# Optimization experiments

Hardware: AMD Instinct MI355X
Metric: run time of the kernel (lower is better)

## Reference

```python
import jax, jax.numpy as jnp
import numpy as np

D_MODEL, FFN, N_EXP = 1024, 4096, 8
BS, L = 4, 2048


def setup_inputs() -> dict:
    key = jax.random.key(0)
    ks = jax.random.split(key, 7)
    s = 0.02
    return {
        "x": jax.random.normal(ks[0], (BS, L, D_MODEL), dtype=jnp.float32),
        "gate_w": s * jax.random.normal(ks[1], (D_MODEL, N_EXP), dtype=jnp.float32),
        "gate_b": jnp.zeros((N_EXP,), dtype=jnp.float32),
        "W1": s * jax.random.normal(ks[2], (N_EXP, D_MODEL, FFN), dtype=jnp.float32),
        "b1": jnp.zeros((N_EXP, FFN), dtype=jnp.float32),
        "W2": s * jax.random.normal(ks[3], (N_EXP, FFN, D_MODEL), dtype=jnp.float32),
        "b2": jnp.zeros((N_EXP, D_MODEL), dtype=jnp.float32),
    }


def reference(x, gate_w, gate_b, W1, b1, W2, b2):
    # gate logits [bs, l, E]; NOTE: original applies Softmax(dim=1) -> over seq dim
    logits = jnp.einsum("bld,de->ble", x, gate_w) + gate_b
    probs = jax.nn.softmax(logits, axis=1)  # faithful to nn.Softmax(dim=1)
    idx = jnp.argmax(probs, axis=-1)  # top-1 expert per token, [bs, l]
    # topk_weights are computed in the original but never applied to output.
    out = jnp.zeros_like(x)
    for e in range(N_EXP):  # fixed small expert loop (structurally distinct weights)
        h = jax.nn.gelu(jnp.einsum("bld,df->blf", x, W1[e]) + b1[e], approximate=False)
        y = jnp.einsum("blf,fd->bld", h, W2[e]) + b2[e]
        out = out + jnp.where((idx == e)[..., None], y, jnp.float32(0.0))
    return out
```

## Files before the change

### kernel.cpp

```cpp
#include <hip/hip_runtime.h>
#include <hip/hip_bf16.h>

typedef unsigned short u16;
typedef unsigned int u32;

using bf16x8 = __attribute__((ext_vector_type(8))) short;
using f32x4  = __attribute__((ext_vector_type(4))) float;

static constexpr int TOK  = 8192;
static constexpr int SEQ  = 2048;
static constexpr int DM   = 1024;
static constexpr int FF   = 4096;
static constexpr int NE   = 8;
static constexpr int MAXT = 72;
static constexpr int MAXT2= 40;
static constexpr int NT2  = DM/128;
static constexpr int KS2  = 2;
static constexpr int NWG1 = MAXT2 * (FF/256);
static constexpr int NWG2 = MAXT * NT2 * KS2;

static constexpr size_t O_LOGITS = 0;
static constexpr size_t O_M      = 262144;
static constexpr size_t O_Z      = O_M + 128;
static constexpr size_t O_CNT    = O_Z + 128;
static constexpr size_t O_CUR    = O_CNT + 64;
static constexpr size_t O_OFF    = O_CUR + 64;
static constexpr size_t O_DESC   = 263168;
static constexpr size_t O_DESC2  = 264320;
static constexpr size_t O_PERM   = 266240;
static constexpr size_t O_IDX    = 299008;
static constexpr size_t O_XG     = 524288;
static constexpr size_t O_W1T    = O_XG  + (size_t)TOK*DM*2;
static constexpr size_t O_W2T    = O_W1T + (size_t)NE*DM*FF*2;
static constexpr size_t O_H      = O_W2T + (size_t)NE*DM*FF*2;

__device__ __forceinline__ u16 f2bf(float f){
  __hip_bfloat16 h = __float2bfloat16(f);
  return *reinterpret_cast<u16*>(&h);
}

__device__ __forceinline__ void gld_lds16(const void* g, void* l){
  __builtin_amdgcn_global_load_lds((const __attribute__((address_space(1))) void*)g,
                                   (__attribute__((address_space(3))) void*)l, 16, 0, 0);
}

#define BAR()    asm volatile("s_barrier" ::: "memory")
#define WAITV0() asm volatile("s_waitcnt vmcnt(0)" ::: "memory")

__device__ __forceinline__ float gelu_f(float v){
  float u = v * fmaf(v*v, 0.044715f, 1.0f) * 0.7978845608f;
  float ex = __builtin_amdgcn_exp2f(u * -2.885390082f);
  return v * __builtin_amdgcn_rcpf(1.0f + ex);
}

__global__ void k_gate(const float* __restrict__ x, const float* __restrict__ gw,
                       const float* __restrict__ gb, float* __restrict__ logits){
  __shared__ float sgw[DM*NE];
  for (int i = threadIdx.x; i < DM*NE; i += 256) sgw[i] = gw[i];
  __syncthreads();
  int wave = threadIdx.x >> 6, lane = threadIdx.x & 63;
  int t = blockIdx.x * 4 + wave;
  const float* xr = x + (size_t)t * DM;
  float acc[NE];
#pragma unroll
  for (int e = 0; e < NE; ++e) acc[e] = 0.f;
#pragma unroll
  for (int k = 0; k < 16; ++k){
    int d = k*64 + lane;
    float xv = xr[d];
    const float* g = &sgw[d*NE];
#pragma unroll
    for (int e = 0; e < NE; ++e) acc[e] = fmaf(xv, g[e], acc[e]);
  }
#pragma unroll
  for (int off = 32; off; off >>= 1)
#pragma unroll
    for (int e = 0; e < NE; ++e) acc[e] += __shfl_xor(acc[e], off);
  if (lane == 0){
#pragma unroll
    for (int e = 0; e < NE; ++e) logits[(size_t)t*NE + e] = acc[e] + gb[e];
  }
}

__global__ void k_lse(const float* __restrict__ logits, float* __restrict__ mOut,
                      float* __restrict__ zOut){
  int be = blockIdx.x;
  int b = be >> 3, e = be & 7;
  const float* base = logits + ((size_t)b*SEQ)*NE + e;
  float m = -INFINITY;
  for (int l = threadIdx.x; l < SEQ; l += 256) m = fmaxf(m, base[(size_t)l*NE]);
  __shared__ float red[8];
#pragma unroll
  for (int off = 32; off; off >>= 1) m = fmaxf(m, __shfl_xor(m, off));
  if ((threadIdx.x & 63) == 0) red[threadIdx.x >> 6] = m;
  __syncthreads();
  m = fmaxf(fmaxf(red[0], red[1]), fmaxf(red[2], red[3]));
  float s = 0.f;
  for (int l = threadIdx.x; l < SEQ; l += 256) s += expf(base[(size_t)l*NE] - m);
#pragma unroll
  for (int off = 32; off; off >>= 1) s += __shfl_xor(s, off);
  if ((threadIdx.x & 63) == 0) red[4 + (threadIdx.x >> 6)] = s;
  __syncthreads();
  if (threadIdx.x == 0){ mOut[be] = m; zOut[be] = red[4]+red[5]+red[6]+red[7]; }
}

__global__ void k_route(const float* __restrict__ logits, const float* __restrict__ m,
                        const float* __restrict__ z, u32* __restrict__ cnt,
                        int* __restrict__ idx){
  int t = blockIdx.x*256 + threadIdx.x;
  int b = t >> 11;
  const float* lr = logits + (size_t)t*NE;
  float best = -INFINITY; int be = 0;
#pragma unroll
  for (int e = 0; e < NE; ++e){
    float p = expf(lr[e] - m[b*NE + e]) / z[b*NE + e];
    if (p > best){ best = p; be = e; }
  }
  idx[t] = be;
  atomicAdd(&cnt[be], 1u);
}

__global__ void k_plan(const u32* __restrict__ cnt, int* __restrict__ off,
                       int4* __restrict__ desc, int4* __restrict__ desc2,
                       u32* __restrict__ cur){
  if (threadIdx.x == 0){
    int offs[NE+1]; int o = 0;
    for (int e = 0; e < NE; ++e){ offs[e] = o; o += (int)cnt[e]; }
    offs[NE] = o;
    int nt = 0, nt2 = 0;
    for (int e = 0; e < NE; ++e){
      int c = (int)cnt[e];
      for (int s = 0; s < c; s += 128)
        desc[nt++] = make_int4(e, offs[e] + s, min(128, c - s), 0);
      for (int s = 0; s < c; s += 256)
        desc2[nt2++] = make_int4(e, offs[e] + s, min(256, c - s), 0);
      off[e] = offs[e]; cur[e] = 0u;
    }
    off[NE] = offs[NE];
    for (int i = nt;  i < MAXT;  ++i) desc[i]  = make_int4(-1, 0, 0, 0);
    for (int i = nt2; i < MAXT2; ++i) desc2[i] = make_int4(-1, 0, 0, 0);
  }
}

__global__ void k_scatter(const int* __restrict__ idx, const int* __restrict__ off,
                          u32* __restrict__ cur, int* __restrict__ perm){
  int t = blockIdx.x*256 + threadIdx.x;
  int e = idx[t];
  int pos = off[e] + (int)atomicAdd(&cur[e], 1u);
  perm[pos] = t;
}

__global__ void k_gather(const float* __restrict__ x, const int* __restrict__ perm,
                         u16* __restrict__ Xg){
  int p = blockIdx.x;
  int t = perm[p];
  const float4* src = (const float4*)(x + (size_t)t*DM);
  float4 v = src[threadIdx.x];
  uint2 o;
  o.x = (u32)f2bf(v.x) | ((u32)f2bf(v.y) << 16);
  o.y = (u32)f2bf(v.z) | ((u32)f2bf(v.w) << 16);
  *(uint2*)(Xg + (size_t)p*DM + threadIdx.x*4) = o;
}

__global__ void k_trans(const float* __restrict__ in, u16* __restrict__ out,
                        int R, int C){
  __shared__ float tile[64][65];
  int e = blockIdx.z;
  int r0 = blockIdx.x*64, c0 = blockIdx.y*64;
  const float* src = in + ((size_t)e*R + r0)*C + c0;
  int lr = threadIdx.x >> 4, lc = (threadIdx.x & 15) * 4;
#pragma unroll
  for (int i = 0; i < 4; ++i){
    float4 v = *(const float4*)(src + (size_t)(lr + i*16)*C + lc);
    tile[lr + i*16][lc+0] = v.x; tile[lr + i*16][lc+1] = v.y;
    tile[lr + i*16][lc+2] = v.z; tile[lr + i*16][lc+3] = v.w;
  }
  __syncthreads();
  u16* dst = out + ((size_t)e*C + c0)*R + r0;
#pragma unroll
  for (int i = 0; i < 4; ++i){
    int oc = lr + i*16;
    u16 a0 = f2bf(tile[lc+0][oc]);
    u16 a1 = f2bf(tile[lc+1][oc]);
    u16 a2 = f2bf(tile[lc+2][oc]);
    u16 a3 = f2bf(tile[lc+3][oc]);
    uint2 o; o.x = (u32)a0 | ((u32)a1 << 16); o.y = (u32)a2 | ((u32)a3 << 16);
    *(uint2*)(dst + (size_t)oc*R + lc) = o;
  }
}

__global__ __launch_bounds__(512, 2) void k_ffn1(const u16* __restrict__ Xg,
    const u16* __restrict__ W1T, const float* __restrict__ b1,
    u16* __restrict__ H, const int4* __restrict__ desc2){
  int pid = blockIdx.x;
  int pid_sw = (pid & 7) * (NWG1/8) + (pid >> 3);
  int mt = pid_sw % MAXT2;
  int n0 = (pid_sw / MAXT2) * 256;
  int4 dd = desc2[mt];
  int e = dd.x; if (e < 0) return;
  int m0 = dd.y, valid = dd.z;

  __shared__ __align__(16) u16 lA[2][256*64];
  __shared__ __align__(16) u16 lB[2][256*64];

  int tid = threadIdx.x, lane = tid & 63, wave = tid >> 6;
  int wm = wave >> 2, wn = wave & 3;
  const u16* Bsrc = W1T + ((size_t)e*FF + n0)*DM;

  f32x4 acc[8][4] = {};
  bf16x8 a[4][2], b0[2][2], b1r[2][2];

  int srow = lane >> 3;
  int cole = ((lane & 7) ^ srow) << 3;

  auto STAGE = [&](int buf, int kt){
    int k0 = kt * 64;
    char* dA = (char*)&lA[buf][0];
    char* dB = (char*)&lB[buf][0];
#pragma unroll
    for (int c = 0; c < 4; ++c){
      int ci = wave*4 + c;
      int row = ci*8 + srow;
      int ra = m0 + row; if (ra > TOK-1) ra = TOK-1;
      gld_lds16(Xg   + (size_t)ra *DM + k0 + cole, dA + ci*1024);
      gld_lds16(Bsrc + (size_t)row*DM + k0 + cole, dB + ci*1024);
    }
  };
  auto LDA = [&](const u16* tb, int half){
#pragma unroll
    for (int f = 0; f < 4; ++f){
      int R = wm*128 + half*64 + f*16 + (lane & 15);
      int base = R*128 + (((lane >> 4)*16) ^ ((R & 7) << 4));
      a[f][0] = *(const bf16x8*)((const char*)tb + base);
      a[f][1] = *(const bf16x8*)((const char*)tb + (base ^ 64));
    }
  };
  auto LDB = [&](const u16* tb, int half, bf16x8 (&b)[2][2]){
#pragma unroll
    for (int f = 0; f < 2; ++f){
      int R = wn*64 + half*32 + f*16 + (lane & 15);
      int base = R*128 + (((lane >> 4)*16) ^ ((R & 7) << 4));
      b[f][0] = *(const bf16x8*)((const char*)tb + base);
      b[f][1] = *(const bf16x8*)((const char*)tb + (base ^ 64));
    }
  };
  auto MM = [&](int mh, int nh, bf16x8 (&b)[2][2]){
    __builtin_amdgcn_s_setprio(1);
#pragma unroll
    for (int f = 0; f < 4; ++f)
#pragma unroll
      for (int g = 0; g < 2; ++g){
        acc[mh*4+f][nh*2+g] =
          __builtin_amdgcn_mfma_f32_16x16x32_bf16(a[f][0], b[g][0], acc[mh*4+f][nh*2+g], 0,0,0);
        acc[mh*4+f][nh*2+g] =
          __builtin_amdgcn_mfma_f32_16x16x32_bf16(a[f][1], b[g][1], acc[mh*4+f][nh*2+g], 0,0,0);
      }
    __builtin_amdgcn_s_setprio(0);
  };

  STAGE(0, 0);
  WAITV0(); BAR();
  const int KT = DM / 64;
  for (int kt = 0; kt < KT; ++kt){
    const u16* cA = &lA[kt & 1][0];
    const u16* cB = &lB[kt & 1][0];
    if (kt + 1 < KT) STAGE((kt & 1) ^ 1, kt + 1);
    LDA(cA, 0); LDB(cB, 0, b0);
    BAR(); MM(0, 0, b0);  BAR();
    LDB(cB, 1, b1r);
    BAR(); MM(0, 1, b1r); BAR();
    LDA(cA, 1);
    BAR(); MM(1, 1, b1r); BAR();
    MM(1, 0, b0);
    if (kt + 1 < KT) WAITV0();
    BAR();
  }

#pragma unroll
  for (int fn = 0; fn < 4; ++fn){
    int col = n0 + wn*64 + fn*16 + (lane & 15);
    float bias = b1[(size_t)e*FF + col];
#pragma unroll
    for (int fm = 0; fm < 8; ++fm){
      int rbase = wm*128 + fm*16 + ((lane >> 4) << 2);
#pragma unroll
      for (int j = 0; j < 4; ++j){
        int rit = rbase + j;
        if (rit < valid){
          float v = acc[fm][fn][j] + bias;
          H[(size_t)(m0 + rit)*FF + col] = f2bf(gelu_f(v));
        }
      }
    }
  }
}

__global__ void k_bias(const int* __restrict__ idx, const float* __restrict__ b2,
                       float* __restrict__ out){
  int t = blockIdx.x;
  int e = idx[t];
  float4 v = *(const float4*)(b2 + (size_t)e*DM + threadIdx.x*4);
  *(float4*)(out + (size_t)t*DM + threadIdx.x*4) = v;
}

__global__ __launch_bounds__(256) void k_ffn2(const u16* __restrict__ H,
    const u16* __restrict__ W2T, float* __restrict__ out,
    const int4* __restrict__ desc, const int* __restrict__ perm){
  int pid = blockIdx.x;
  int pid_sw = (pid & 7) * (NWG2/8) + (pid >> 3);
  int mt = pid_sw % MAXT;
  int rest = pid_sw / MAXT;
  int n0 = (rest & 7) * 128;
  int ks = rest >> 3;
  int4 dd = desc[mt];
  int e = dd.x; if (e < 0) return;
  int m0 = dd.y, valid = dd.z;
  __shared__ __align__(16) u16 lA[2][128*32];
  __shared__ __align__(16) u16 lB[2][128*32];
  int tid = threadIdx.x, lane = tid & 63, wave = tid >> 6;
  int wr = wave >> 1, wc = wave & 1;
  const u16* Bsrc = W2T + ((size_t)e*DM + n0)*FF;
  f32x4 acc[4][4] = {};

  auto stage = [&](int buf, int kt){
    int k0 = kt * 32;
#pragma unroll
    for (int i = 0; i < 2; ++i){
      int qbase = wave*512 + i*2048;
      int qe = qbase + lane*8;
      int row = qe >> 5, col = qe & 31;
      int rowg = m0 + row; if (rowg > TOK-1) rowg = TOK-1;
      gld_lds16(H + (size_t)rowg*FF + k0 + col, &lA[buf][qbase]);
      gld_lds16(Bsrc + (size_t)row*FF + k0 + col, &lB[buf][qbase]);
    }
  };

  const int k_beg = ks * 64, k_end = k_beg + 64;
  stage(0, k_beg);
  __syncthreads();
  for (int kt = k_beg; kt < k_end; ++kt){
    int cur = kt & 1;
    if (kt + 1 < k_end) stage(cur ^ 1, kt + 1);
    const u16* pa = &lA[cur][(wr*64 + (lane & 15))*32 + (lane >> 4)*8];
    const u16* pb = &lB[cur][(wc*64 + (lane & 15))*32 + (lane >> 4)*8];
    bf16x8 a[4], b[4];
#pragma unroll
    for (int m = 0; m < 4; ++m) a[m] = *(const bf16x8*)(pa + m*16*32);
#pragma unroll
    for (int n = 0; n < 4; ++n) b[n] = *(const bf16x8*)(pb + n*16*32);
#pragma unroll
    for (int m = 0; m < 4; ++m)
#pragma unroll
      for (int n = 0; n < 4; ++n)
        acc[m][n] = __builtin_amdgcn_mfma_f32_16x16x32_bf16(a[m], b[n], acc[m][n], 0, 0, 0);
    __syncthreads();
  }

#pragma unroll
  for (int m = 0; m < 4; ++m){
#pragma unroll
    for (int j = 0; j < 4; ++j){
      int rit = wr*64 + m*16 + ((lane >> 4) << 2) + j;
      if (rit < valid){
        int tok = perm[m0 + rit];
#pragma unroll
        for (int n = 0; n < 4; ++n){
          int col = n0 + wc*64 + n*16 + (lane & 15);
          unsafeAtomicAdd(&out[(size_t)tok*DM + col], acc[m][n][j]);
        }
      }
    }
  }
}

extern "C" void kernel_launch(void* const* d_in, const int* in_sizes, int n_in,
                              void* d_out, int out_size, void* d_ws, size_t ws_size,
                              hipStream_t stream){
  const float* x   = (const float*)d_in[0];
  const float* gw  = (const float*)d_in[1];
  const float* gb  = (const float*)d_in[2];
  const float* W1  = (const float*)d_in[3];
  const float* b1  = (const float*)d_in[4];
  const float* W2  = (const float*)d_in[5];
  const float* b2  = (const float*)d_in[6];
  float* out = (float*)d_out;
  char* ws = (char*)d_ws;

  float* logits = (float*)(ws + O_LOGITS);
  float* mArr   = (float*)(ws + O_M);
  float* zArr   = (float*)(ws + O_Z);
  u32*   cnt    = (u32*)  (ws + O_CNT);
  u32*   cur    = (u32*)  (ws + O_CUR);
  int*   off    = (int*)  (ws + O_OFF);
  int4*  desc   = (int4*) (ws + O_DESC);
  int4*  desc2  = (int4*) (ws + O_DESC2);
  int*   perm   = (int*)  (ws + O_PERM);
  int*   idx    = (int*)  (ws + O_IDX);
  u16*   Xg     = (u16*)  (ws + O_XG);
  u16*   W1T    = (u16*)  (ws + O_W1T);
  u16*   W2T    = (u16*)  (ws + O_W2T);
  u16*   Hbuf   = (u16*)  (ws + O_H);

  hipMemsetAsync(ws + O_CNT, 0, 128, stream);

  k_gate   <<<TOK/4, 256, 0, stream>>>(x, gw, gb, logits);
  k_lse    <<<32,    256, 0, stream>>>(logits, mArr, zArr);
  k_route  <<<TOK/256, 256, 0, stream>>>(logits, mArr, zArr, cnt, idx);
  k_plan   <<<1,     64,  0, stream>>>(cnt, off, desc, desc2, cur);
  k_scatter<<<TOK/256, 256, 0, stream>>>(idx, off, cur, perm);
  k_gather <<<TOK,   256, 0, stream>>>(x, perm, Xg);
  k_trans  <<<dim3(DM/64, FF/64, NE), 256, 0, stream>>>(W1, W1T, DM, FF);
  k_trans  <<<dim3(FF/64, DM/64, NE), 256, 0, stream>>>(W2, W2T, FF, DM);
  k_ffn1   <<<NWG1,  512, 0, stream>>>(Xg, W1T, b1, Hbuf, desc2);
  k_bias   <<<TOK,   256, 0, stream>>>(idx, b2, out);
  k_ffn2   <<<NWG2,  256, 0, stream>>>(Hbuf, W2T, out, desc, perm);
}
```

Before: 548.7 us.

## Port ffn2 to 256x256 tiled 8-wave kernel and simplify ffn1 inner loop

Rewrites the second expert GEMM to use the same 256x256x64 swizzled LDS tiling, 512-thread, two-blocks-per-CU structure as the first GEMM. It uses the coarser 256-row tile descriptors and a 4-way K split in place of 128x128 tiles with a 2-way split. The first GEMM's inner loop now loads all B fragments once per K step and drops the intermediate barriers. The goal is more data reuse per tile and fewer synchronisation points. The cost is higher register pressure, and the extra K split doubles the atomic adds to the output.

New measurement: 555.5 us. No clear change (+1.2%).

```diff
diff --git a/kernel.cpp b/kernel.cpp
--- a/kernel.cpp
+++ b/kernel.cpp
@@ -14,10 +14,9 @@
 static constexpr int NE   = 8;
 static constexpr int MAXT = 72;
 static constexpr int MAXT2= 40;
-static constexpr int NT2  = DM/128;
-static constexpr int KS2  = 2;
+static constexpr int KS2  = 4;
 static constexpr int NWG1 = MAXT2 * (FF/256);
-static constexpr int NWG2 = MAXT * NT2 * KS2;
+static constexpr int NWG2 = MAXT2 * (DM/256) * KS2;
 
 static constexpr size_t O_LOGITS = 0;
 static constexpr size_t O_M      = 262144;
@@ -189,6 +188,7 @@
   }
 }
 
+
 __global__ __launch_bounds__(512, 2) void k_ffn1(const u16* __restrict__ Xg,
     const u16* __restrict__ W1T, const float* __restrict__ b1,
     u16* __restrict__ H, const int4* __restrict__ desc2){
@@ -208,7 +208,7 @@
   const u16* Bsrc = W1T + ((size_t)e*FF + n0)*DM;
 
   f32x4 acc[8][4] = {};
-  bf16x8 a[4][2], b0[2][2], b1r[2][2];
+  bf16x8 a[4][2], b[4][2];
 
   int srow = lane >> 3;
   int cole = ((lane & 7) ^ srow) << 3;
@@ -235,25 +235,25 @@
       a[f][1] = *(const bf16x8*)((const char*)tb + (base ^ 64));
     }
   };
-  auto LDB = [&](const u16* tb, int half, bf16x8 (&b)[2][2]){
-#pragma unroll
-    for (int f = 0; f < 2; ++f){
-      int R = wn*64 + half*32 + f*16 + (lane & 15);
+  auto LDB = [&](const u16* tb){
+#pragma unroll
+    for (int f = 0; f < 4; ++f){
+      int R = wn*64 + f*16 + (lane & 15);
       int base = R*128 + (((lane >> 4)*16) ^ ((R & 7) << 4));
       b[f][0] = *(const bf16x8*)((const char*)tb + base);
       b[f][1] = *(const bf16x8*)((const char*)tb + (base ^ 64));
     }
   };
-  auto MM = [&](int mh, int nh, bf16x8 (&b)[2][2]){
+  auto MM = [&](int half){
     __builtin_amdgcn_s_setprio(1);
 #pragma unroll
     for (int f = 0; f < 4; ++f)
 #pragma unroll
-      for (int g = 0; g < 2; ++g){
-        acc[mh*4+f][nh*2+g] =
-          __builtin_amdgcn_mfma_f32_16x16x32_bf16(a[f][0], b[g][0], acc[mh*4+f][nh*2+g], 0,0,0);
-        acc[mh*4+f][nh*2+g] =
-          __builtin_amdgcn_mfma_f32_16x16x32_bf16(a[f][1], b[g][1], acc[mh*4+f][nh*2+g], 0,0,0);
+      for (int g = 0; g < 4; ++g){
+        acc[half*4+f][g] =
+          __builtin_amdgcn_mfma_f32_16x16x32_bf16(a[f][0], b[g][0], acc[half*4+f][g], 0,0,0);
+        acc[half*4+f][g] =
+          __builtin_amdgcn_mfma_f32_16x16x32_bf16(a[f][1], b[g][1], acc[half*4+f][g], 0,0,0);
       }
     __builtin_amdgcn_s_setprio(0);
   };
@@ -262,17 +262,16 @@
   WAITV0(); BAR();
   const int KT = DM / 64;
   for (int kt = 0; kt < KT; ++kt){
-    const u16* cA = &lA[kt & 1][0];
-    const u16* cB = &lB[kt & 1][0];
-    if (kt + 1 < KT) STAGE((kt & 1) ^ 1, kt + 1);
-    LDA(cA, 0); LDB(cB, 0, b0);
-    BAR(); MM(0, 0, b0);  BAR();
-    LDB(cB, 1, b1r);
-    BAR(); MM(0, 1, b1r); BAR();
+    int cur = kt & 1;
+    const u16* cA = &lA[cur][0];
+    const u16* cB = &lB[cur][0];
+    if (kt + 1 < KT) STAGE(cur ^ 1, kt + 1);
+    LDB(cB);
+    LDA(cA, 0);
+    MM(0);
     LDA(cA, 1);
-    BAR(); MM(1, 1, b1r); BAR();
-    MM(1, 0, b0);
-    if (kt + 1 < KT) WAITV0();
+    MM(1);
+    WAITV0();
     BAR();
   }
 
@@ -303,70 +302,106 @@
   *(float4*)(out + (size_t)t*DM + threadIdx.x*4) = v;
 }
 
-__global__ __launch_bounds__(256) void k_ffn2(const u16* __restrict__ H,
+__global__ __launch_bounds__(512, 2) void k_ffn2(const u16* __restrict__ H,
     const u16* __restrict__ W2T, float* __restrict__ out,
-    const int4* __restrict__ desc, const int* __restrict__ perm){
+    const int4* __restrict__ desc2, const int* __restrict__ perm){
   int pid = blockIdx.x;
   int pid_sw = (pid & 7) * (NWG2/8) + (pid >> 3);
-  int mt = pid_sw % MAXT;
-  int rest = pid_sw / MAXT;
-  int n0 = (rest & 7) * 128;
-  int ks = rest >> 3;
-  int4 dd = desc[mt];
+  int mt = pid_sw % MAXT2;
+  int rest = pid_sw / MAXT2;
+  int n0 = (rest & 3) * 256;
+  int ks = rest >> 2;
+  int4 dd = desc2[mt];
   int e = dd.x; if (e < 0) return;
   int m0 = dd.y, valid = dd.z;
-  __shared__ __align__(16) u16 lA[2][128*32];
-  __shared__ __align__(16) u16 lB[2][128*32];
+
+  __shared__ __align__(16) u16 lA[2][256*64];
+  __shared__ __align__(16) u16 lB[2][256*64];
+
   int tid = threadIdx.x, lane = tid & 63, wave = tid >> 6;
-  int wr = wave >> 1, wc = wave & 1;
+  int wm = wave >> 2, wn = wave & 3;
   const u16* Bsrc = W2T + ((size_t)e*DM + n0)*FF;
-  f32x4 acc[4][4] = {};
-
-  auto stage = [&](int buf, int kt){
-    int k0 = kt * 32;
-#pragma unroll
-    for (int i = 0; i < 2; ++i){
-      int qbase = wave*512 + i*2048;
-      int qe = qbase + lane*8;
-      int row = qe >> 5, col = qe & 31;
-      int rowg = m0 + row; if (rowg > TOK-1) rowg = TOK-1;
-      gld_lds16(H + (size_t)rowg*FF + k0 + col, &lA[buf][qbase]);
-      gld_lds16(Bsrc + (size_t)row*FF + k0 + col, &lB[buf][qbase]);
-    }
-  };
-
-  const int k_beg = ks * 64, k_end = k_beg + 64;
-  stage(0, k_beg);
-  __syncthreads();
-  for (int kt = k_beg; kt < k_end; ++kt){
+  const int kbase = ks * (FF/KS2);
+
+  f32x4 acc[8][4] = {};
+  bf16x8 a[4][2], b[4][2];
+
+  int srow = lane >> 3;
+  int cole = ((lane & 7) ^ srow) << 3;
+
+  auto STAGE = [&](int buf, int kt){
+    int k0 = kbase + kt * 64;
+    char* dA = (char*)&lA[buf][0];
+    char* dB = (char*)&lB[buf][0];
+#pragma unroll
+    for (int c = 0; c < 4; ++c){
+      int ci = wave*4 + c;
+      int row = ci*8 + srow;
+      int ra = m0 + row; if (ra > TOK-1) ra = TOK-1;
+      gld_lds16(H    + (size_t)ra *FF + k0 + cole, dA + ci*1024);
+      gld_lds16(Bsrc + (size_t)row*FF + k0 + cole, dB + ci*1024);
+    }
+  };
+  auto LDA = [&](const u16* tb, int half){
+#pragma unroll
+    for (int f = 0; f < 4; ++f){
+      int R = wm*128 + half*64 + f*16 + (lane & 15);
+      int base = R*128 + (((lane >> 4)*16) ^ ((R & 7) << 4));
+      a[f][0] = *(const bf16x8*)((const char*)tb + base);
+      a[f][1] = *(const bf16x8*)((const char*)tb + (base ^ 64));
+    }
+  };
+  auto LDB = [&](const u16* tb){
+#pragma unroll
+    for (int f = 0; f < 4; ++f){
+      int R = wn*64 + f*16 + (lane & 15);
+      int base = R*128 + (((lane >> 4)*16) ^ ((R & 7) << 4));
+      b[f][0] = *(const bf16x8*)((const char*)tb + base);
+      b[f][1] = *(const bf16x8*)((const char*)tb + (base ^ 64));
+    }
+  };
+  auto MM = [&](int half){
+    __builtin_amdgcn_s_setprio(1);
+#pragma unroll
+    for (int f = 0; f < 4; ++f)
+#pragma unroll
+      for (int g = 0; g < 4; ++g){
+        acc[half*4+f][g] =
+          __builtin_amdgcn_mfma_f32_16x16x32_bf16(a[f][0], b[g][0], acc[half*4+f][g], 0,0,0);
+        acc[half*4+f][g] =
+          __builtin_amdgcn_mfma_f32_16x16x32_bf16(a[f][1], b[g][1], acc[half*4+f][g], 0,0,0);
+      }
+    __builtin_amdgcn_s_setprio(0);
+  };
+
+  STAGE(0, 0);
+  WAITV0(); BAR();
+  const int KT = (FF/KS2) / 64;
+  for (int kt = 0; kt < KT; ++kt){
     int cur = kt & 1;
-    if (kt + 1 < k_end) stage(cur ^ 1, kt + 1);
-    const u16* pa = &lA[cur][(wr*64 + (lane & 15))*32 + (lane >> 4)*8];
-    const u16* pb = &lB[cur][(wc*64 + (lane & 15))*32 + (lane >> 4)*8];
-    bf16x8 a[4], b[4];
-#pragma unroll
-    for (int m = 0; m < 4; ++m) a[m] = *(const bf16x8*)(pa + m*16*32);
-#pragma unroll
-    for (int n = 0; n < 4; ++n) b[n] = *(const bf16x8*)(pb + n*16*32);
-#pragma unroll
-    for (int m = 0; m < 4; ++m)
-#pragma unroll
-      for (int n = 0; n < 4; ++n)
-        acc[m][n] = __builtin_amdgcn_mfma_f32_16x16x32_bf16(a[m], b[n], acc[m][n], 0, 0, 0);
-    __syncthreads();
-  }
-
-#pragma unroll
-  for (int m = 0; m < 4; ++m){
+    const u16* cA = &lA[cur][0];
+    const u16* cB = &lB[cur][0];
+    if (kt + 1 < KT) STAGE(cur ^ 1, kt + 1);
+    LDB(cB);
+    LDA(cA, 0);
+    MM(0);
+    LDA(cA, 1);
+    MM(1);
+    WAITV0();
+    BAR();
+  }
+
+#pragma unroll
+  for (int fm = 0; fm < 8; ++fm){
 #pragma unroll
     for (int j = 0; j < 4; ++j){
-      int rit = wr*64 + m*16 + ((lane >> 4) << 2) + j;
+      int rit = wm*128 + fm*16 + ((lane >> 4) << 2) + j;
       if (rit < valid){
         int tok = perm[m0 + rit];
 #pragma unroll
-        for (int n = 0; n < 4; ++n){
-          int col = n0 + wc*64 + n*16 + (lane & 15);
-          unsafeAtomicAdd(&out[(size_t)tok*DM + col], acc[m][n][j]);
+        for (int fn = 0; fn < 4; ++fn){
+          int col = n0 + wn*64 + fn*16 + (lane & 15);
+          unsafeAtomicAdd(&out[(size_t)tok*DM + col], acc[fm][fn][j]);
         }
       }
     }
@@ -413,5 +448,5 @@
   k_trans  <<<dim3(FF/64, DM/64, NE), 256, 0, stream>>>(W2, W2T, FF, DM);
   k_ffn1   <<<NWG1,  512, 0, stream>>>(Xg, W1T, b1, Hbuf, desc2);
   k_bias   <<<TOK,   256, 0, stream>>>(idx, b2, out);
-  k_ffn2   <<<NWG2,  256, 0, stream>>>(Hbuf, W2T, out, desc, perm);
-}
+  k_ffn2   <<<NWG2,  512, 0, stream>>>(Hbuf, W2T, out, desc2, perm);
+}
```
